# Kernel tuning notes

Hardware: AMD Instinct MI355X
Metric: run time of the kernel (lower is better)

The kernel has to match this reference:

```python
import jax, jax.numpy as jnp
import numpy as np
import math

NUM_HEADS = 16
HEAD_SIZE = 64
QKT_MEAN = 0.0
QKT_STD = 0.05
APPLY_NOISE = True
NOISE_KEY = jax.random.key(42)


def quantize_activation_8bit(x):
    max_abs = jnp.maximum(jnp.max(jnp.abs(x)), 1e-08)
    scale = max_abs / 127.0
    return jnp.clip(jnp.round(x / scale), -127, 127) * scale


def quantize_weight_4bit(w):
    max_abs = jnp.maximum(jnp.max(jnp.abs(w)), 1e-08)
    scale = max_abs / 7.0
    return jnp.clip(jnp.round(w / scale), -7, 7) * scale


def setup_inputs() -> dict:
    key = jax.random.key(0)
    k1, k2, k3, k4 = jax.random.split(key, 4)
    B, S, D = 4, 1024, 1024
    hidden_states = jax.random.normal(k1, (B, S, D), dtype=jnp.float32)
    attention_mask = jnp.zeros((B, 1, 1, S), dtype=jnp.float32)
    # nn.Linear weights are [out_features, in_features]
    w_scale = 1.0 / math.sqrt(D)
    Wq = jax.random.normal(k2, (D, D), dtype=jnp.float32) * w_scale
    Wk = jax.random.normal(k3, (D, D), dtype=jnp.float32) * w_scale
    Wv = jax.random.normal(k4, (D, D), dtype=jnp.float32) * w_scale
    return {"hidden_states": hidden_states, "attention_mask": attention_mask,
            "Wq": Wq, "Wk": Wk, "Wv": Wv}


def _split_heads(x):
    B, S, _ = x.shape
    return x.reshape(B, S, NUM_HEADS, HEAD_SIZE).transpose(0, 2, 1, 3)  # [B,H,S,Dh]


def reference(hidden_states, attention_mask, Wq, Wk, Wv):
    h_q = quantize_activation_8bit(hidden_states)
    h_k = quantize_activation_8bit(hidden_states)
    Q = _split_heads(jnp.einsum('bsd,od->bso', h_q, quantize_weight_4bit(Wq)))
    K = _split_heads(jnp.einsum('bsd,od->bso', h_k, quantize_weight_4bit(Wk)))
    V = _split_heads(jnp.einsum('bsd,od->bso', hidden_states, quantize_weight_4bit(Wv)))
    qkt = jnp.einsum('bhqd,bhkd->bhqk', Q, K) / math.sqrt(HEAD_SIZE)
    if APPLY_NOISE and QKT_STD > 0:
        noise = jax.random.normal(NOISE_KEY, qkt.shape, dtype=qkt.dtype) * QKT_STD + QKT_MEAN
        qkt = qkt + noise
    qkt = qkt + attention_mask  # [B,1,1,S] broadcasts over [B,H,S,S]
    attn_weights = jax.nn.softmax(qkt, axis=-1)  # dropout is identity in eval
    ctx = jnp.einsum('bhqk,bhkd->bhqd', attn_weights, V)
    B, H, S, Dh = ctx.shape
    ctx = ctx.transpose(0, 2, 1, 3).reshape(B, S, H * Dh)
    return ctx
```

## Files before the change

kernel.cpp:

```cpp
#include <hip/hip_runtime.h>
#include <hip/hip_bf16.h>

typedef unsigned short u16;
typedef unsigned int u32;
typedef __bf16 bf16x8 __attribute__((ext_vector_type(8)));
typedef __bf16 bf16x4 __attribute__((ext_vector_type(4)));
typedef float f32x4 __attribute__((ext_vector_type(4)));

#define MFMA16(a, b, c) __builtin_amdgcn_mfma_f32_16x16x32_bf16((a), (b), (c), 0, 0, 0)

#define GLOAD_LDS16(gp, lp)                                        \
    __builtin_amdgcn_global_load_lds(                              \
        (const __attribute__((address_space(1))) void*)(gp),       \
        (__attribute__((address_space(3))) void*)(lp), 16, 0, 0)

static __device__ __forceinline__ u32 f2bfbits(float f) {
    union { float f; u32 u; } c; c.f = f;
    return (c.u + 0x7FFFu + ((c.u >> 16) & 1u)) >> 16;
}
static __device__ __forceinline__ u32 f2bfbits_exact(float f) {
    union { float f; u32 u; } c; c.f = f;
    return c.u >> 16;
}
static __device__ __forceinline__ u32 pack_bf16x2(float lo, float hi) {
    float2 v; v.x = lo; v.y = hi;
    union { __hip_bfloat162 h; u32 u; } c;
    c.h = __float22bfloat162_rn(v);
    return c.u;
}

static __device__ __forceinline__ u32 rotl_ab(u32 x, int r) {
    return __builtin_amdgcn_alignbit(x, x, 32 - r);
}

static __device__ __forceinline__ float exp2_fast(float x) {
    float r;
    asm("v_exp_f32 %0, %1\n\ts_nop 1" : "=v"(r) : "v"(x));
    return r;
}

static __device__ __forceinline__ void noise_pu8(u32 tk, float* __restrict__ pu) {
    const u32 K1 = 42u, K2 = 0x1BD11BF0u;
    u32 x0[8], x1[8];
#pragma unroll
    for (int d = 0; d < 8; d++) {
        u32 a = tk + (u32)(d < 4 ? d : 12 + d);
        x0[d] = a;
        x1[d] = rotl_ab(a, 13) ^ a;
    }
#define TFR(R)                                             \
    _Pragma("unroll") for (int d = 0; d < 8; d++) {        \
        x0[d] += x1[d];                                    \
        x1[d] = rotl_ab(x1[d], R) ^ x0[d];                 \
    }
#define TFRI(R, A, B)                                      \
    _Pragma("unroll") for (int d = 0; d < 8; d++) {        \
        x1[d] += (B);                                      \
        x0[d] += (A) + x1[d];              \
        x1[d] = rotl_ab(x1[d], R) ^ x0[d];                 \
    }
    TFR(15) TFR(26) TFR(6)
    TFRI(17, K1, K2 + 1u) TFR(29) TFR(16) TFR(24)
    TFRI(13, K2, 2u)      TFR(15) TFR(26) TFR(6)
    TFRI(17, 0u, K1 + 3u) TFR(29) TFR(16) TFR(24)
    TFRI(13, K1, K2 + 4u) TFR(15) TFR(26) TFR(6)
#undef TFR
#undef TFRI
#pragma unroll
    for (int d = 0; d < 8; d++) {
        u32 bits = (x0[d] + K2) ^ (x1[d] + 5u);
        u32 vb = __builtin_amdgcn_alignbit(0x80u, bits, 9);
        float v2 = __uint_as_float(vb);
        float u = v2 - 3.0f;
        float t = fmaf(-u, u, 1.0f);
        float L2 = __log2f(t);
        L2 = fmaxf(L2, -7.2134752f);
        float z = fmaf(L2, -0.69314718f, -2.5f);
        float p = 2.81022636e-08f;
        p = fmaf(p, z, 3.43273939e-07f);
        p = fmaf(p, z, -3.5233877e-06f);
        p = fmaf(p, z, -4.39150654e-06f);
        p = fmaf(p, z, 0.00021858087f);
        p = fmaf(p, z, -0.00125372503f);
        p = fmaf(p, z, -0.00417768164f);
        p = fmaf(p, z, 0.246640727f);
        p = fmaf(p, z, 1.50140941f);
        pu[d] = p * u;
    }
}

__global__ __launch_bounds__(256) void absmax_k(const float* __restrict__ h,
                                                const float* __restrict__ wq,
                                                const float* __restrict__ wk,
                                                const float* __restrict__ wv,
                                                u32* __restrict__ slots) {
    int t = blockIdx.y;
    const float* src = (t == 0) ? h : (t == 1) ? wq : (t == 2) ? wk : wv;
    int n4 = ((t == 0) ? 4096 * 1024 : 1024 * 1024) / 4;
    u32 mx = 0;
    int tid = threadIdx.x;
    for (int i = blockIdx.x * blockDim.x + tid; i < n4; i += gridDim.x * blockDim.x) {
        uint4 v = ((const uint4*)src)[i];
        mx = max(mx, v.x & 0x7FFFFFFFu);
        mx = max(mx, v.y & 0x7FFFFFFFu);
        mx = max(mx, v.z & 0x7FFFFFFFu);
        mx = max(mx, v.w & 0x7FFFFFFFu);
    }
    __shared__ u32 red[256];
    red[tid] = mx;
    __syncthreads();
    for (int s = 128; s > 0; s >>= 1) {
        if (tid < s) red[tid] = max(red[tid], red[tid + s]);
        __syncthreads();
    }
    if (tid == 0) atomicMax(&slots[t], red[0]);
}

__global__ __launch_bounds__(256) void prequant_all(const float* __restrict__ hidden,
                                                    const float* __restrict__ wq,
                                                    const float* __restrict__ wk,
                                                    const float* __restrict__ wv,
                                                    u16* __restrict__ hq,
                                                    u16* __restrict__ hbf,
                                                    u16* __restrict__ wqi,
                                                    u16* __restrict__ wki,
                                                    u16* __restrict__ wvi,
                                                    const u32* __restrict__ slots) {
    int y = blockIdx.y;
    const float* src = (y == 0) ? hidden : (y == 1) ? wq : (y == 2) ? wk : wv;
    u16* dqi = (y == 0) ? hq : (y == 1) ? wqi : (y == 2) ? wki : wvi;
    u16* draw = (y == 0) ? hbf : nullptr;
    float qmax = (y == 0) ? 127.0f : 7.0f;
    int n8 = ((y == 0) ? 4096 * 1024 : 1024 * 1024) / 8;

    float amax = fmaxf(__uint_as_float(slots[y]), 1e-8f);
    float scale = amax / qmax;
    for (int i = blockIdx.x * blockDim.x + threadIdx.x; i < n8; i += gridDim.x * blockDim.x) {
        float4 a = ((const float4*)src)[2 * i];
        float4 b = ((const float4*)src)[2 * i + 1];
        float x[8] = {a.x, a.y, a.z, a.w, b.x, b.y, b.z, b.w};
        u16 qi[8], rw[8];
#pragma unroll
        for (int j = 0; j < 8; j++) {
            float q = fminf(fmaxf(rintf(x[j] / scale), -qmax), qmax);
            qi[j] = (u16)f2bfbits_exact(q);
            rw[j] = (u16)f2bfbits(x[j]);
        }
        *(uint4*)(dqi + 8 * (size_t)i) = *(const uint4*)qi;
        if (draw) *(uint4*)(draw + 8 * (size_t)i) = *(const uint4*)rw;
    }
}

__global__ __launch_bounds__(256, 2) void qkv_gemm_all(const u16* __restrict__ hq,
                                                       const u16* __restrict__ hbf,
                                                       const u16* __restrict__ wqi,
                                                       const u16* __restrict__ wki,
                                                       const u16* __restrict__ wvi,
                                                       const u32* __restrict__ slots,
                                                       u16* __restrict__ Qb,
                                                       u16* __restrict__ Kb,
                                                       u16* __restrict__ Vtb) {
    __shared__ __align__(16) u16 As[128 * 32];
    __shared__ __align__(16) u16 Bs[128 * 32];
    int z = blockIdx.z;
    const u16* A  = (z < 2) ? hq : hbf;
    const u16* Bw = (z == 0) ? wqi : (z == 1) ? wki : wvi;
    u16* outp     = (z == 0) ? Qb : (z == 1) ? Kb : Vtb;
    int transOut = (z == 2);
    float s_a = fmaxf(__uint_as_float(slots[0]), 1e-8f) / 127.0f;
    float s_w = fmaxf(__uint_as_float(slots[z + 1]), 1e-8f) / 7.0f;
    float oscale = (z < 2) ? (s_a * s_w) : s_w;

    int tid = threadIdx.x;
    int mbase = blockIdx.x * 128, nbase = blockIdx.y * 128;
    int lane = tid & 63, w = tid >> 6;
    int wv_m = w & 1, wv_n = w >> 1;
    int quad = lane >> 4, l16 = lane & 15;

    int srow = lane >> 2, scol = (lane & 3) * 8;
    const u16* ag0 = A + (size_t)(mbase + w * 32 + srow) * 1024 + scol;
    const u16* ag1 = A + (size_t)(mbase + w * 32 + 16 + srow) * 1024 + scol;
    const u16* bg0 = Bw + (size_t)(nbase + w * 32 + srow) * 1024 + scol;
    const u16* bg1 = Bw + (size_t)(nbase + w * 32 + 16 + srow) * 1024 + scol;
    u16* al0 = As + w * 1024;
    u16* al1 = As + w * 1024 + 512;
    u16* bl0 = Bs + w * 1024;
    u16* bl1 = Bs + w * 1024 + 512;

    f32x4 acc[4][4];
#pragma unroll
    for (int i = 0; i < 4; i++)
#pragma unroll
        for (int j = 0; j < 4; j++) acc[i][j] = (f32x4){0.f, 0.f, 0.f, 0.f};

    for (int k0 = 0; k0 < 1024; k0 += 32) {
        __syncthreads();
        GLOAD_LDS16(ag0 + k0, al0);
        GLOAD_LDS16(ag1 + k0, al1);
        GLOAD_LDS16(bg0 + k0, bl0);
        GLOAD_LDS16(bg1 + k0, bl1);
        __syncthreads();

        bf16x8 af[4], bfr[4];
#pragma unroll
        for (int mt = 0; mt < 4; mt++)
            af[mt] = *(const bf16x8*)(As + (wv_m * 64 + mt * 16 + l16) * 32 + quad * 8);
#pragma unroll
        for (int nt = 0; nt < 4; nt++)
            bfr[nt] = *(const bf16x8*)(Bs + (wv_n * 64 + nt * 16 + l16) * 32 + quad * 8);
#pragma unroll
        for (int mt = 0; mt < 4; mt++)
#pragma unroll
            for (int nt = 0; nt < 4; nt++)
                acc[mt][nt] = MFMA16(af[mt], bfr[nt], acc[mt][nt]);
    }

#pragma unroll
    for (int mt = 0; mt < 4; mt++)
#pragma unroll
        for (int nt = 0; nt < 4; nt++)
#pragma unroll
            for (int r = 0; r < 4; r++) {
                float val = acc[mt][nt][r] * oscale;
                int m = mbase + wv_m * 64 + mt * 16 + quad * 4 + r;
                int o = nbase + wv_n * 64 + nt * 16 + l16;
                int b = m >> 10, s = m & 1023;
                int hh = o >> 6, dh = o & 63;
                size_t off = transOut ? (((size_t)(b * 16 + hh) * 64 + dh) * 1024 + s)
                                      : (((size_t)(b * 16 + hh) * 1024 + s) * 64 + dh);
                outp[off] = (u16)f2bfbits(val);
            }
}

__global__ __launch_bounds__(256, 4) void attn_kernel(const u16* __restrict__ Q,
                                                      const u16* __restrict__ K,
                                                      const u16* __restrict__ Vt,
                                                      const float* __restrict__ mask,
                                                      float* __restrict__ O0,
                                                      float* __restrict__ O1,
                                                      float* __restrict__ l0,
                                                      float* __restrict__ l1) {
    __shared__ __align__(16) u16 Ks[2][32 * 64];
    __shared__ __align__(16) u16 Vs[2][64 * 32];
    __shared__ __align__(16) float msk2[512];

    int qt = blockIdx.x, h = blockIdx.y;
    int b = blockIdx.z & 3, split = blockIdx.z >> 2;
    int bh = b * 16 + h;
    int tid = threadIdx.x, wv = tid >> 6, lane = tid & 63;
    int quad = lane >> 4, l16 = lane & 15;
    int q0 = qt * 64 + wv * 16;
    int ks0 = split * 512;

    const float IL2 = 1.4426950408889634f;
    const float C_S = 0.18033688011112042f;
    const float C_N = 0.10201394645f;

    const float* maskb = mask + b * 1024 + ks0;
    msk2[tid] = maskb[tid] * IL2;
    msk2[tid + 256] = maskb[tid + 256] * IL2;

    float* Obuf = split ? O1 : O0;
    float* lbuf = split ? l1 : l0;
    const u16* Qb = Q + (size_t)bh * 1024 * 64;
    const u16* Kb = K + (size_t)bh * 1024 * 64;
    const u16* Vb = Vt + (size_t)bh * 64 * 1024 + ks0;

    bf16x8 aq0 = *(const bf16x8*)(Qb + (q0 + l16) * 64 + quad * 8);
    bf16x8 aq1 = *(const bf16x8*)(Qb + (q0 + l16) * 64 + 32 + quad * 8);

    union { u32 u[4]; bf16x8 v; } ones;
#pragma unroll
    for (int i = 0; i < 4; i++) ones.u[i] = 0x3F803F80u;

    f32x4 oacc[4];
#pragma unroll
    for (int i = 0; i < 4; i++) oacc[i] = (f32x4){0.f, 0.f, 0.f, 0.f};
    f32x4 lacc = (f32x4){0.f, 0.f, 0.f, 0.f};

    u32 tbase = ((u32)(bh * 1024 + q0 + l16)) * 1024u + (u32)ks0 + (u32)(4 * quad) + 42u;

    const u16* kgsrc = Kb + (size_t)(ks0 + wv * 8 + (lane >> 3)) * 64 + (lane & 7) * 8;
    const u16* vgsrc = Vb + (size_t)(wv * 16 + (lane >> 2)) * 1024 + (lane & 3) * 8;
    u16* kdst0 = &Ks[0][wv * 512];
    u16* kdst1 = &Ks[1][wv * 512];
    u16* vdst0 = &Vs[0][wv * 512];
    u16* vdst1 = &Vs[1][wv * 512];

    GLOAD_LDS16(kgsrc, kdst0);
    GLOAD_LDS16(vgsrc, vdst0);
    __syncthreads();

    for (int kk = 0; kk < 512; kk += 32) {
        int cur = (kk >> 5) & 1;
        if (kk + 32 < 512) {
            GLOAD_LDS16(kgsrc + (kk + 32) * 64, cur ? kdst0 : kdst1);
            GLOAD_LDS16(vgsrc + (kk + 32),     cur ? vdst0 : vdst1);
        }
        const u16* Kc = cur ? Ks[1] : Ks[0];
        const u16* Vc = cur ? Vs[1] : Vs[0];

        f32x4 mk4 = *(const f32x4*)(msk2 + kk + 4 * quad);
        f32x4 mh4 = *(const f32x4*)(msk2 + kk + 16 + 4 * quad);

        float pu[8];
        noise_pu8(tbase + (u32)kk, pu);

        bf16x8 bk0 = *(const bf16x8*)(Kc + l16 * 64 + quad * 8);
        bf16x8 bk1 = *(const bf16x8*)(Kc + l16 * 64 + 32 + quad * 8);
        bf16x8 bk2 = *(const bf16x8*)(Kc + (16 + l16) * 64 + quad * 8);
        bf16x8 bk3 = *(const bf16x8*)(Kc + (16 + l16) * 64 + 32 + quad * 8);

        f32x4 s0 = (f32x4){0.f, 0.f, 0.f, 0.f};
        f32x4 s1 = (f32x4){0.f, 0.f, 0.f, 0.f};
        s0 = MFMA16(bk0, aq0, s0);
        s0 = MFMA16(bk1, aq1, s0);
        s1 = MFMA16(bk2, aq0, s1);
        s1 = MFMA16(bk3, aq1, s1);

        float e[8];
#pragma unroll
        for (int r = 0; r < 4; r++) {
            e[r]     = exp2_fast(fmaf(pu[r],     C_N, fmaf(s0[r], C_S, mk4[r])));
            e[4 + r] = exp2_fast(fmaf(pu[4 + r], C_N, fmaf(s1[r], C_S, mh4[r])));
        }
        union { u32 u[4]; bf16x8 v; } pf;
        pf.u[0] = pack_bf16x2(e[0], e[1]);
        pf.u[1] = pack_bf16x2(e[2], e[3]);
        pf.u[2] = pack_bf16x2(e[4], e[5]);
        pf.u[3] = pack_bf16x2(e[6], e[7]);

#pragma unroll
        for (int nt = 0; nt < 4; nt++) {
            bf16x4 vlo = *(const bf16x4*)(Vc + (nt * 16 + l16) * 32 + quad * 4);
            bf16x4 vhi = *(const bf16x4*)(Vc + (nt * 16 + l16) * 32 + 16 + quad * 4);
            bf16x8 vf = __builtin_shufflevector(vlo, vhi, 0, 1, 2, 3, 4, 5, 6, 7);
            oacc[nt] = MFMA16(pf.v, vf, oacc[nt]);
        }
        lacc = MFMA16(pf.v, ones.v, lacc);

        __syncthreads();
    }

    if (l16 == 0) {
        int lbase = bh * 1024 + q0 + quad * 4;
#pragma unroll
        for (int r = 0; r < 4; r++) lbuf[lbase + r] = lacc[r];
    }
#pragma unroll
    for (int nt = 0; nt < 4; nt++) {
#pragma unroll
        for (int r = 0; r < 4; r++) {
            int q = q0 + quad * 4 + r;
            int dh = nt * 16 + l16;
            Obuf[((size_t)(b * 1024 + q)) * 1024 + h * 64 + dh] = oacc[nt][r];
        }
    }
}

__global__ __launch_bounds__(256) void combine_k(float* __restrict__ outp,
                                                 const float* __restrict__ O1,
                                                 const float* __restrict__ l0,
                                                 const float* __restrict__ l1) {
    int gid = blockIdx.x * 256 + threadIdx.x;
    int e = gid << 2;
    int bq = e >> 10;
    int h = (e & 1023) >> 6;
    int b = bq >> 10, q = bq & 1023;
    int lidx = ((b * 16 + h) << 10) + q;
    float linv = 1.0f / (l0[lidx] + l1[lidx]);
    float4 a = ((const float4*)outp)[gid];
    float4 c = ((const float4*)O1)[gid];
    float4 o;
    o.x = (a.x + c.x) * linv;
    o.y = (a.y + c.y) * linv;
    o.z = (a.z + c.z) * linv;
    o.w = (a.w + c.w) * linv;
    ((float4*)outp)[gid] = o;
}

extern "C" void kernel_launch(void* const* d_in, const int* in_sizes, int n_in,
                              void* d_out, int out_size, void* d_ws, size_t ws_size,
                              hipStream_t stream) {
    (void)in_sizes; (void)n_in; (void)out_size; (void)ws_size;
    const float* hidden = (const float*)d_in[0];
    const float* maskp  = (const float*)d_in[1];
    const float* Wq     = (const float*)d_in[2];
    const float* Wk     = (const float*)d_in[3];
    const float* Wv     = (const float*)d_in[4];
    float* outp = (float*)d_out;

    char* ws = (char*)d_ws;
    u32* slots = (u32*)ws;
    u16* hq  = (u16*)(ws + 256);
    u16* hbf = hq + 4096 * 1024;
    u16* wqi = hbf + 4096 * 1024;
    u16* wki = wqi + 1024 * 1024;
    u16* wvi = wki + 1024 * 1024;
    u16* Qb  = wvi + 1024 * 1024;
    u16* Kb  = Qb + 4096 * 1024;
    u16* Vtb = Kb + 4096 * 1024;

    float* O1buf = (float*)hq;
    float* l0buf = (float*)wqi;
    float* l1buf = l0buf + 4 * 16 * 1024;

    hipMemsetAsync(slots, 0, 16, stream);
    absmax_k<<<dim3(128, 4), 256, 0, stream>>>(hidden, Wq, Wk, Wv, slots);
    prequant_all<<<dim3(64, 4), 256, 0, stream>>>(hidden, Wq, Wk, Wv,
                                                  hq, hbf, wqi, wki, wvi, slots);
    qkv_gemm_all<<<dim3(32, 8, 3), 256, 0, stream>>>(hq, hbf, wqi, wki, wvi, slots,
                                                     Qb, Kb, Vtb);
    attn_kernel<<<dim3(16, 16, 8), 256, 0, stream>>>(Qb, Kb, Vtb, maskp,
                                                     outp, O1buf, l0buf, l1buf);
    combine_k<<<dim3(4096), 256, 0, stream>>>(outp, O1buf, l0buf, l1buf);
}
```

Before: 345.3 us.

## Drop split-K attention and normalize output inside attention kernel

Removes the two-way split over the key dimension in the attention kernel so each block processes all 1024 keys, and normalizes by the row sum directly in the epilogue. This eliminates the combine kernel launch, the partial O1/l buffers and their extra global traffic. In exchange the grid halves to 1024 blocks with twice the serial loop length per block, which reduces available parallelism and latency hiding.

```diff
diff --git a/kernel.cpp b/kernel.cpp
--- a/kernel.cpp
+++ b/kernel.cpp
@@ -236,35 +236,31 @@
                                                       const u16* __restrict__ K,
                                                       const u16* __restrict__ Vt,
                                                       const float* __restrict__ mask,
-                                                      float* __restrict__ O0,
-                                                      float* __restrict__ O1,
-                                                      float* __restrict__ l0,
-                                                      float* __restrict__ l1) {
+                                                      float* __restrict__ outp) {
     __shared__ __align__(16) u16 Ks[2][32 * 64];
     __shared__ __align__(16) u16 Vs[2][64 * 32];
-    __shared__ __align__(16) float msk2[512];
+    __shared__ __align__(16) float msk2[1024];
 
     int qt = blockIdx.x, h = blockIdx.y;
-    int b = blockIdx.z & 3, split = blockIdx.z >> 2;
+    int b = blockIdx.z;
     int bh = b * 16 + h;
     int tid = threadIdx.x, wv = tid >> 6, lane = tid & 63;
     int quad = lane >> 4, l16 = lane & 15;
     int q0 = qt * 64 + wv * 16;
-    int ks0 = split * 512;
 
     const float IL2 = 1.4426950408889634f;
     const float C_S = 0.18033688011112042f;
     const float C_N = 0.10201394645f;
 
-    const float* maskb = mask + b * 1024 + ks0;
+    const float* maskb = mask + b * 1024;
     msk2[tid] = maskb[tid] * IL2;
     msk2[tid + 256] = maskb[tid + 256] * IL2;
-
-    float* Obuf = split ? O1 : O0;
-    float* lbuf = split ? l1 : l0;
+    msk2[tid + 512] = maskb[tid + 512] * IL2;
+    msk2[tid + 768] = maskb[tid + 768] * IL2;
+
     const u16* Qb = Q + (size_t)bh * 1024 * 64;
     const u16* Kb = K + (size_t)bh * 1024 * 64;
-    const u16* Vb = Vt + (size_t)bh * 64 * 1024 + ks0;
+    const u16* Vb = Vt + (size_t)bh * 64 * 1024;
 
     bf16x8 aq0 = *(const bf16x8*)(Qb + (q0 + l16) * 64 + quad * 8);
     bf16x8 aq1 = *(const bf16x8*)(Qb + (q0 + l16) * 64 + 32 + quad * 8);
@@ -278,9 +274,9 @@
     for (int i = 0; i < 4; i++) oacc[i] = (f32x4){0.f, 0.f, 0.f, 0.f};
     f32x4 lacc = (f32x4){0.f, 0.f, 0.f, 0.f};
 
-    u32 tbase = ((u32)(bh * 1024 + q0 + l16)) * 1024u + (u32)ks0 + (u32)(4 * quad) + 42u;
-
-    const u16* kgsrc = Kb + (size_t)(ks0 + wv * 8 + (lane >> 3)) * 64 + (lane & 7) * 8;
+    u32 tbase = ((u32)(bh * 1024 + q0 + l16)) * 1024u + (u32)(4 * quad) + 42u;
+
+    const u16* kgsrc = Kb + (size_t)(wv * 8 + (lane >> 3)) * 64 + (lane & 7) * 8;
     const u16* vgsrc = Vb + (size_t)(wv * 16 + (lane >> 2)) * 1024 + (lane & 3) * 8;
     u16* kdst0 = &Ks[0][wv * 512];
     u16* kdst1 = &Ks[1][wv * 512];
@@ -291,9 +287,9 @@
     GLOAD_LDS16(vgsrc, vdst0);
     __syncthreads();
 
-    for (int kk = 0; kk < 512; kk += 32) {
+    for (int kk = 0; kk < 1024; kk += 32) {
         int cur = (kk >> 5) & 1;
-        if (kk + 32 < 512) {
+        if (kk + 32 < 1024) {
             GLOAD_LDS16(kgsrc + (kk + 32) * 64, cur ? kdst0 : kdst1);
             GLOAD_LDS16(vgsrc + (kk + 32),     cur ? vdst0 : vdst1);
         }
@@ -342,41 +338,15 @@
         __syncthreads();
     }
 
-    if (l16 == 0) {
-        int lbase = bh * 1024 + q0 + quad * 4;
-#pragma unroll
-        for (int r = 0; r < 4; r++) lbuf[lbase + r] = lacc[r];
-    }
-#pragma unroll
-    for (int nt = 0; nt < 4; nt++) {
-#pragma unroll
-        for (int r = 0; r < 4; r++) {
-            int q = q0 + quad * 4 + r;
-            int dh = nt * 16 + l16;
-            Obuf[((size_t)(b * 1024 + q)) * 1024 + h * 64 + dh] = oacc[nt][r];
-        }
-    }
-}
-
-__global__ __launch_bounds__(256) void combine_k(float* __restrict__ outp,
-                                                 const float* __restrict__ O1,
-                                                 const float* __restrict__ l0,
-                                                 const float* __restrict__ l1) {
-    int gid = blockIdx.x * 256 + threadIdx.x;
-    int e = gid << 2;
-    int bq = e >> 10;
-    int h = (e & 1023) >> 6;
-    int b = bq >> 10, q = bq & 1023;
-    int lidx = ((b * 16 + h) << 10) + q;
-    float linv = 1.0f / (l0[lidx] + l1[lidx]);
-    float4 a = ((const float4*)outp)[gid];
-    float4 c = ((const float4*)O1)[gid];
-    float4 o;
-    o.x = (a.x + c.x) * linv;
-    o.y = (a.y + c.y) * linv;
-    o.z = (a.z + c.z) * linv;
-    o.w = (a.w + c.w) * linv;
-    ((float4*)outp)[gid] = o;
+#pragma unroll
+    for (int r = 0; r < 4; r++) {
+        float linv = 1.0f / lacc[r];
+        int q = q0 + quad * 4 + r;
+        float* orow = outp + ((size_t)(b * 1024 + q)) * 1024 + h * 64;
+#pragma unroll
+        for (int nt = 0; nt < 4; nt++)
+            orow[nt * 16 + l16] = oacc[nt][r] * linv;
+    }
 }
 
 extern "C" void kernel_launch(void* const* d_in, const int* in_sizes, int n_in,
@@ -401,17 +371,11 @@
     u16* Kb  = Qb + 4096 * 1024;
     u16* Vtb = Kb + 4096 * 1024;
 
-    float* O1buf = (float*)hq;
-    float* l0buf = (float*)wqi;
-    float* l1buf = l0buf + 4 * 16 * 1024;
-
     hipMemsetAsync(slots, 0, 16, stream);
     absmax_k<<<dim3(128, 4), 256, 0, stream>>>(hidden, Wq, Wk, Wv, slots);
     prequant_all<<<dim3(64, 4), 256, 0, stream>>>(hidden, Wq, Wk, Wv,
                                                   hq, hbf, wqi, wki, wvi, slots);
     qkv_gemm_all<<<dim3(32, 8, 3), 256, 0, stream>>>(hq, hbf, wqi, wki, wvi, slots,
                                                      Qb, Kb, Vtb);
-    attn_kernel<<<dim3(16, 16, 8), 256, 0, stream>>>(Qb, Kb, Vtb, maskp,
-                                                     outp, O1buf, l0buf, l1buf);
-    combine_k<<<dim3(4096), 256, 0, stream>>>(outp, O1buf, l0buf, l1buf);
-}
+    attn_kernel<<<dim3(16, 16, 4), 256, 0, stream>>>(Qb, Kb, Vtb, maskp, outp);
+}
```

Result: no change. 350.5 us (+1.5%).
